# Performance work log

Hardware: AMD Instinct MI355X
Metric: run time of the kernel (lower is better)

Reference implementation:

```python
import jax, jax.numpy as jnp
import numpy as np

BOUND = 1.0
NUM_STEPS = 128
MIN_NEAR = 0.05


def setup_inputs() -> dict:
    key = jax.random.key(0)
    ks = jax.random.split(key, 7)
    B, N, H = 2, 8192, 64
    # camera origins on a radius-2 sphere, rays aimed at jittered points near origin
    o = jax.random.normal(ks[0], (B, N, 3), jnp.float32)
    o = 2.0 * o / (jnp.linalg.norm(o, axis=-1, keepdims=True) + 1e-8)
    tgt = 0.5 * jax.random.normal(ks[1], (B, N, 3), jnp.float32)
    d = tgt - o
    d = d / (jnp.linalg.norm(d, axis=-1, keepdims=True) + 1e-8)
    W1 = jax.random.normal(ks[2], (3, H), jnp.float32) * 0.5
    W2 = jax.random.normal(ks[3], (3, H), jnp.float32) * 0.5
    b1 = jax.random.normal(ks[4], (H,), jnp.float32) * 0.1
    w_sigma = jax.random.normal(ks[5], (H, 1), jnp.float32) * 0.5
    W_color = jax.random.normal(ks[6], (H, 3), jnp.float32) * 0.5
    return {"rays_o": o, "rays_d": d, "W1": W1, "W2": W2, "b1": b1,
            "w_sigma": w_sigma, "W_color": W_color}


def _near_far(rays_o, rays_d):
    # cube AABB intersection (near_far_from_bound, type='cube')
    inv = 1.0 / (rays_d + 1e-15)
    tmin = (-BOUND - rays_o) * inv
    tmax = (BOUND - rays_o) * inv
    near = jnp.max(jnp.minimum(tmin, tmax), axis=-1, keepdims=True)  # [B,N,1]
    far = jnp.min(jnp.maximum(tmin, tmax), axis=-1, keepdims=True)
    miss = far < near
    near = jnp.where(miss, 1e9, near)
    far = jnp.where(miss, 1e9, far)
    near = jnp.maximum(near, MIN_NEAR)
    return near, far


def reference(rays_o, rays_d, W1, W2, b1, w_sigma, W_color):
    nears, fars = _near_far(rays_o, rays_d)                    # [B,N,1]
    t = jnp.linspace(0.0, 1.0, NUM_STEPS, dtype=jnp.float32)   # [S]
    z_vals = nears + (fars - nears) * t                        # [B,N,S]
    sample_dist = (fars - nears) / (NUM_STEPS - 1)             # [B,N,1]

    # sample points along rays, clamped to the AABB
    xyzs = rays_o[..., None, :] + rays_d[..., None, :] * z_vals[..., None]  # [B,N,S,3]
    xyzs = jnp.clip(xyzs, -BOUND, BOUND)

    # network stub: tiny per-sample MLP -> sigma [B,N,S], color [B,N,S,3]
    h = jax.nn.relu(jnp.einsum('bnsc,ch->bnsh', xyzs, W1)
                    + jnp.einsum('bnc,ch->bnh', rays_d, W2)[:, :, None, :]
                    + b1)
    sigma = jax.nn.softplus(jnp.einsum('bnsh,ho->bnso', h, w_sigma))[..., 0]
    rgbs = jax.nn.sigmoid(jnp.einsum('bnsh,hc->bnsc', h, W_color))

    # alpha compositing
    deltas = z_vals[..., 1:] - z_vals[..., :-1]                # [B,N,S-1]
    deltas = jnp.concatenate([deltas, sample_dist], axis=-1)   # [B,N,S]
    alphas = 1.0 - jnp.exp(-deltas * sigma)
    alphas_shifted = jnp.concatenate(
        [jnp.ones_like(alphas[..., :1]), 1.0 - alphas + 1e-15], axis=-1)
    weights = alphas * jnp.cumprod(alphas_shifted, axis=-1)[..., :-1]  # [B,N,S]

    weights_sum = weights.sum(axis=-1)                         # [B,N]
    depth = jnp.sum(weights * z_vals, axis=-1)                 # [B,N]
    image = jnp.sum(weights[..., None] * rgbs, axis=-2)        # [B,N,3], bg_color=0
    return image, depth, weights, weights_sum
```

## Files before the change

### kernel.cpp

```cpp
#include <hip/hip_runtime.h>
#include <math.h>

#define NSTEPS 128
#define HID 64
#define RAYS_PER_BLOCK 8
#define SAMPLES_PER_THREAD 4

__global__ __launch_bounds__(256) void nerf_render_kernel(
    const float* __restrict__ rays_o,
    const float* __restrict__ rays_d,
    const float* __restrict__ W1,
    const float* __restrict__ W2,
    const float* __restrict__ b1,
    const float* __restrict__ w_sigma,
    const float* __restrict__ W_color,
    float* __restrict__ out_image,
    float* __restrict__ out_depth,
    float* __restrict__ out_weights,
    float* __restrict__ out_wsum,
    int R)
{
    __shared__ float wl[HID][12];
    const int tid = threadIdx.x;
    if (tid < HID) {
        const int j = tid;
        wl[j][0]  = W1[0 * HID + j];
        wl[j][1]  = W1[1 * HID + j];
        wl[j][2]  = W1[2 * HID + j];
        wl[j][3]  = W2[0 * HID + j];
        wl[j][4]  = W2[1 * HID + j];
        wl[j][5]  = W2[2 * HID + j];
        wl[j][6]  = b1[j];
        wl[j][7]  = w_sigma[j];
        wl[j][8]  = W_color[j * 3 + 0];
        wl[j][9]  = W_color[j * 3 + 1];
        wl[j][10] = W_color[j * 3 + 2];
        wl[j][11] = 0.0f;
    }
    __syncthreads();

    const int r   = tid >> 5;
    const int l   = tid & 31;
    const int ray = blockIdx.x * RAYS_PER_BLOCK + r;
    if (ray >= R) return;

    const float o0 = rays_o[ray * 3 + 0];
    const float o1 = rays_o[ray * 3 + 1];
    const float o2 = rays_o[ray * 3 + 2];
    const float d0 = rays_d[ray * 3 + 0];
    const float d1 = rays_d[ray * 3 + 1];
    const float d2 = rays_d[ray * 3 + 2];

    const float inv0 = 1.0f / (d0 + 1e-15f);
    const float inv1 = 1.0f / (d1 + 1e-15f);
    const float inv2 = 1.0f / (d2 + 1e-15f);
    const float t0a = (-1.0f - o0) * inv0, t0b = (1.0f - o0) * inv0;
    const float t1a = (-1.0f - o1) * inv1, t1b = (1.0f - o1) * inv1;
    const float t2a = (-1.0f - o2) * inv2, t2b = (1.0f - o2) * inv2;
    float near = fmaxf(fmaxf(fminf(t0a, t0b), fminf(t1a, t1b)), fminf(t2a, t2b));
    float far  = fminf(fminf(fmaxf(t0a, t0b), fmaxf(t1a, t1b)), fmaxf(t2a, t2b));
    if (far < near) { near = 1e9f; far = 1e9f; }
    near = fmaxf(near, 0.05f);
    const float span = far - near;
    const float sample_dist = span * (1.0f / (NSTEPS - 1));

    float z[SAMPLES_PER_THREAD];
    float x0[SAMPLES_PER_THREAD], x1[SAMPLES_PER_THREAD], x2[SAMPLES_PER_THREAD];
#pragma unroll
    for (int k = 0; k < SAMPLES_PER_THREAD; k++) {
        const int s = l * SAMPLES_PER_THREAD + k;
        const float t = (float)s * (1.0f / (NSTEPS - 1));
        z[k] = near + span * t;
        x0[k] = fminf(fmaxf(fmaf(d0, z[k], o0), -1.0f), 1.0f);
        x1[k] = fminf(fmaxf(fmaf(d1, z[k], o1), -1.0f), 1.0f);
        x2[k] = fminf(fmaxf(fmaf(d2, z[k], o2), -1.0f), 1.0f);
    }

    float aS[SAMPLES_PER_THREAD] = {0.f, 0.f, 0.f, 0.f};
    float aR[SAMPLES_PER_THREAD] = {0.f, 0.f, 0.f, 0.f};
    float aG[SAMPLES_PER_THREAD] = {0.f, 0.f, 0.f, 0.f};
    float aB[SAMPLES_PER_THREAD] = {0.f, 0.f, 0.f, 0.f};

#pragma unroll 8
    for (int j = 0; j < HID; j++) {
        const float4 A  = *(const float4*)&wl[j][0];
        const float4 Bq = *(const float4*)&wl[j][4];
        const float4 Cq = *(const float4*)&wl[j][8];
        const float base = fmaf(d0, A.w, fmaf(d1, Bq.x, fmaf(d2, Bq.y, Bq.z)));
#pragma unroll
        for (int k = 0; k < SAMPLES_PER_THREAD; k++) {
            float h = fmaf(x0[k], A.x, fmaf(x1[k], A.y, fmaf(x2[k], A.z, base)));
            h = fmaxf(h, 0.0f);
            aS[k] = fmaf(h, Bq.w, aS[k]);
            aR[k] = fmaf(h, Cq.x, aR[k]);
            aG[k] = fmaf(h, Cq.y, aG[k]);
            aB[k] = fmaf(h, Cq.z, aB[k]);
        }
    }

    float alpha[SAMPLES_PER_THREAD], Tloc[SAMPLES_PER_THREAD];
    float pl = 1.0f;
#pragma unroll
    for (int k = 0; k < SAMPLES_PER_THREAD; k++) {
        const float x = aS[k];
        const float sig = fmaxf(x, 0.0f) + log1pf(expf(-fabsf(x)));
        alpha[k] = 1.0f - expf(-sample_dist * sig);
        Tloc[k] = pl;
        pl *= (1.0f - alpha[k] + 1e-15f);
    }

    float inc = pl;
#pragma unroll
    for (int dlt = 1; dlt < 32; dlt <<= 1) {
        const float v = __shfl_up(inc, dlt, 32);
        if (l >= dlt) inc *= v;
    }
    float excl = __shfl_up(inc, 1, 32);
    if (l == 0) excl = 1.0f;

    float w[SAMPLES_PER_THREAD];
    float wsum = 0.f, dep = 0.f, im0 = 0.f, im1 = 0.f, im2 = 0.f;
#pragma unroll
    for (int k = 0; k < SAMPLES_PER_THREAD; k++) {
        const float T  = excl * Tloc[k];
        const float wt = alpha[k] * T;
        w[k] = wt;
        wsum += wt;
        dep  += wt * z[k];
        const float cr = 1.0f / (1.0f + expf(-aR[k]));
        const float cg = 1.0f / (1.0f + expf(-aG[k]));
        const float cb = 1.0f / (1.0f + expf(-aB[k]));
        im0 += wt * cr;
        im1 += wt * cg;
        im2 += wt * cb;
    }

    *(float4*)&out_weights[(size_t)ray * NSTEPS + l * SAMPLES_PER_THREAD] =
        make_float4(w[0], w[1], w[2], w[3]);

#pragma unroll
    for (int dlt = 16; dlt >= 1; dlt >>= 1) {
        wsum += __shfl_down(wsum, dlt, 32);
        dep  += __shfl_down(dep,  dlt, 32);
        im0  += __shfl_down(im0,  dlt, 32);
        im1  += __shfl_down(im1,  dlt, 32);
        im2  += __shfl_down(im2,  dlt, 32);
    }
    if (l == 0) {
        out_image[ray * 3 + 0] = im0;
        out_image[ray * 3 + 1] = im1;
        out_image[ray * 3 + 2] = im2;
        out_depth[ray] = dep;
        out_wsum[ray]  = wsum;
    }
}

extern "C" void kernel_launch(void* const* d_in, const int* in_sizes, int n_in,
                              void* d_out, int out_size, void* d_ws, size_t ws_size,
                              hipStream_t stream) {
    const float* rays_o  = (const float*)d_in[0];
    const float* rays_d  = (const float*)d_in[1];
    const float* W1      = (const float*)d_in[2];
    const float* W2      = (const float*)d_in[3];
    const float* b1      = (const float*)d_in[4];
    const float* w_sigma = (const float*)d_in[5];
    const float* W_color = (const float*)d_in[6];

    const int R = in_sizes[0] / 3;

    float* out         = (float*)d_out;
    float* out_image   = out;
    float* out_depth   = out_image + (size_t)R * 3;
    float* out_weights = out_depth + R;
    float* out_wsum    = out_weights + (size_t)R * NSTEPS;

    const int blocks = (R + RAYS_PER_BLOCK - 1) / RAYS_PER_BLOCK;
    nerf_render_kernel<<<blocks, 256, 0, stream>>>(
        rays_o, rays_d, W1, W2, b1, w_sigma, W_color,
        out_image, out_depth, out_weights, out_wsum, R);
}
```

Measured before the change: 105.2 us.

## Read MLP weights from global memory directly, drop LDS staging and barrier

```diff
diff --git a/kernel.cpp b/kernel.cpp
--- a/kernel.cpp
+++ b/kernel.cpp
@@ -6,7 +6,7 @@
 #define RAYS_PER_BLOCK 8
 #define SAMPLES_PER_THREAD 4
 
-__global__ __launch_bounds__(256) void nerf_render_kernel(
+__global__ __launch_bounds__(256, 6) void nerf_render_kernel(
     const float* __restrict__ rays_o,
     const float* __restrict__ rays_d,
     const float* __restrict__ W1,
@@ -20,29 +20,12 @@
     float* __restrict__ out_wsum,
     int R)
 {
-    __shared__ float wl[HID][12];
     const int tid = threadIdx.x;
-    if (tid < HID) {
-        const int j = tid;
-        wl[j][0]  = W1[0 * HID + j];
-        wl[j][1]  = W1[1 * HID + j];
-        wl[j][2]  = W1[2 * HID + j];
-        wl[j][3]  = W2[0 * HID + j];
-        wl[j][4]  = W2[1 * HID + j];
-        wl[j][5]  = W2[2 * HID + j];
-        wl[j][6]  = b1[j];
-        wl[j][7]  = w_sigma[j];
-        wl[j][8]  = W_color[j * 3 + 0];
-        wl[j][9]  = W_color[j * 3 + 1];
-        wl[j][10] = W_color[j * 3 + 2];
-        wl[j][11] = 0.0f;
-    }
-    __syncthreads();
-
     const int r   = tid >> 5;
     const int l   = tid & 31;
-    const int ray = blockIdx.x * RAYS_PER_BLOCK + r;
-    if (ray >= R) return;
+    int ray = blockIdx.x * RAYS_PER_BLOCK + r;
+    const bool valid = (ray < R);
+    if (!valid) ray = R - 1;
 
     const float o0 = rays_o[ray * 3 + 0];
     const float o1 = rays_o[ray * 3 + 1];
@@ -64,16 +47,15 @@
     const float span = far - near;
     const float sample_dist = span * (1.0f / (NSTEPS - 1));
 
-    float z[SAMPLES_PER_THREAD];
     float x0[SAMPLES_PER_THREAD], x1[SAMPLES_PER_THREAD], x2[SAMPLES_PER_THREAD];
 #pragma unroll
     for (int k = 0; k < SAMPLES_PER_THREAD; k++) {
         const int s = l * SAMPLES_PER_THREAD + k;
         const float t = (float)s * (1.0f / (NSTEPS - 1));
-        z[k] = near + span * t;
-        x0[k] = fminf(fmaxf(fmaf(d0, z[k], o0), -1.0f), 1.0f);
-        x1[k] = fminf(fmaxf(fmaf(d1, z[k], o1), -1.0f), 1.0f);
-        x2[k] = fminf(fmaxf(fmaf(d2, z[k], o2), -1.0f), 1.0f);
+        const float z = fmaf(span, t, near);
+        x0[k] = fminf(fmaxf(fmaf(d0, z, o0), -1.0f), 1.0f);
+        x1[k] = fminf(fmaxf(fmaf(d1, z, o1), -1.0f), 1.0f);
+        x2[k] = fminf(fmaxf(fmaf(d2, z, o2), -1.0f), 1.0f);
     }
 
     float aS[SAMPLES_PER_THREAD] = {0.f, 0.f, 0.f, 0.f};
@@ -81,20 +63,43 @@
     float aG[SAMPLES_PER_THREAD] = {0.f, 0.f, 0.f, 0.f};
     float aB[SAMPLES_PER_THREAD] = {0.f, 0.f, 0.f, 0.f};
 
-#pragma unroll 8
-    for (int j = 0; j < HID; j++) {
-        const float4 A  = *(const float4*)&wl[j][0];
-        const float4 Bq = *(const float4*)&wl[j][4];
-        const float4 Cq = *(const float4*)&wl[j][8];
-        const float base = fmaf(d0, A.w, fmaf(d1, Bq.x, fmaf(d2, Bq.y, Bq.z)));
+    for (int jc = 0; jc < HID; jc += 4) {
+        const float4 w1x = *(const float4*)&W1[0 * HID + jc];
+        const float4 w1y = *(const float4*)&W1[1 * HID + jc];
+        const float4 w1z = *(const float4*)&W1[2 * HID + jc];
+        const float4 w2x = *(const float4*)&W2[0 * HID + jc];
+        const float4 w2y = *(const float4*)&W2[1 * HID + jc];
+        const float4 w2z = *(const float4*)&W2[2 * HID + jc];
+        const float4 bb  = *(const float4*)&b1[jc];
+        const float4 ws  = *(const float4*)&w_sigma[jc];
+        const float4 wc0 = *(const float4*)&W_color[jc * 3 + 0];
+        const float4 wc1 = *(const float4*)&W_color[jc * 3 + 4];
+        const float4 wc2 = *(const float4*)&W_color[jc * 3 + 8];
+
+        const float c1x[4] = {w1x.x, w1x.y, w1x.z, w1x.w};
+        const float c1y[4] = {w1y.x, w1y.y, w1y.z, w1y.w};
+        const float c1z[4] = {w1z.x, w1z.y, w1z.z, w1z.w};
+        const float c2x[4] = {w2x.x, w2x.y, w2x.z, w2x.w};
+        const float c2y[4] = {w2y.x, w2y.y, w2y.z, w2y.w};
+        const float c2z[4] = {w2z.x, w2z.y, w2z.z, w2z.w};
+        const float cb[4]  = {bb.x, bb.y, bb.z, bb.w};
+        const float cs[4]  = {ws.x, ws.y, ws.z, ws.w};
+        const float ccr[4] = {wc0.x, wc0.w, wc1.z, wc2.y};
+        const float ccg[4] = {wc0.y, wc1.x, wc1.w, wc2.z};
+        const float ccb[4] = {wc0.z, wc1.y, wc2.x, wc2.w};
+
 #pragma unroll
-        for (int k = 0; k < SAMPLES_PER_THREAD; k++) {
-            float h = fmaf(x0[k], A.x, fmaf(x1[k], A.y, fmaf(x2[k], A.z, base)));
-            h = fmaxf(h, 0.0f);
-            aS[k] = fmaf(h, Bq.w, aS[k]);
-            aR[k] = fmaf(h, Cq.x, aR[k]);
-            aG[k] = fmaf(h, Cq.y, aG[k]);
-            aB[k] = fmaf(h, Cq.z, aB[k]);
+        for (int u = 0; u < 4; u++) {
+            const float base = fmaf(d0, c2x[u], fmaf(d1, c2y[u], fmaf(d2, c2z[u], cb[u])));
+#pragma unroll
+            for (int k = 0; k < SAMPLES_PER_THREAD; k++) {
+                float h = fmaf(x0[k], c1x[u], fmaf(x1[k], c1y[u], fmaf(x2[k], c1z[u], base)));
+                h = fmaxf(h, 0.0f);
+                aS[k] = fmaf(h, cs[u],  aS[k]);
+                aR[k] = fmaf(h, ccr[u], aR[k]);
+                aG[k] = fmaf(h, ccg[u], aG[k]);
+                aB[k] = fmaf(h, ccb[u], aB[k]);
+            }
         }
     }
 
@@ -103,8 +108,8 @@
 #pragma unroll
     for (int k = 0; k < SAMPLES_PER_THREAD; k++) {
         const float x = aS[k];
-        const float sig = fmaxf(x, 0.0f) + log1pf(expf(-fabsf(x)));
-        alpha[k] = 1.0f - expf(-sample_dist * sig);
+        const float sig = fmaxf(x, 0.0f) + __logf(1.0f + __expf(-fabsf(x)));
+        alpha[k] = 1.0f - __expf(-sample_dist * sig);
         Tloc[k] = pl;
         pl *= (1.0f - alpha[k] + 1e-15f);
     }
@@ -122,21 +127,26 @@
     float wsum = 0.f, dep = 0.f, im0 = 0.f, im1 = 0.f, im2 = 0.f;
 #pragma unroll
     for (int k = 0; k < SAMPLES_PER_THREAD; k++) {
+        const int s = l * SAMPLES_PER_THREAD + k;
+        const float t = (float)s * (1.0f / (NSTEPS - 1));
+        const float z = fmaf(span, t, near);
         const float T  = excl * Tloc[k];
         const float wt = alpha[k] * T;
         w[k] = wt;
         wsum += wt;
-        dep  += wt * z[k];
-        const float cr = 1.0f / (1.0f + expf(-aR[k]));
-        const float cg = 1.0f / (1.0f + expf(-aG[k]));
-        const float cb = 1.0f / (1.0f + expf(-aB[k]));
+        dep  += wt * z;
+        const float cr = 1.0f / (1.0f + __expf(-aR[k]));
+        const float cg = 1.0f / (1.0f + __expf(-aG[k]));
+        const float cb2 = 1.0f / (1.0f + __expf(-aB[k]));
         im0 += wt * cr;
         im1 += wt * cg;
-        im2 += wt * cb;
+        im2 += wt * cb2;
     }
 
-    *(float4*)&out_weights[(size_t)ray * NSTEPS + l * SAMPLES_PER_THREAD] =
-        make_float4(w[0], w[1], w[2], w[3]);
+    if (valid) {
+        *(float4*)&out_weights[(size_t)ray * NSTEPS + l * SAMPLES_PER_THREAD] =
+            make_float4(w[0], w[1], w[2], w[3]);
+    }
 
 #pragma unroll
     for (int dlt = 16; dlt >= 1; dlt >>= 1) {
@@ -146,7 +156,7 @@
         im1  += __shfl_down(im1,  dlt, 32);
         im2  += __shfl_down(im2,  dlt, 32);
     }
-    if (l == 0) {
+    if (l == 0 && valid) {
         out_image[ray * 3 + 0] = im0;
         out_image[ray * 3 + 1] = im1;
         out_image[ray * 3 + 2] = im2;
```

Measured after the change: 97.40 us. 7.4% less time.
